# Optimization experiments

Hardware: AMD Instinct MI355X
Metric: run time of the kernel (lower is better)

The kernel has to match this reference:

```python
import jax, jax.numpy as jnp
import numpy as np

N_NODES = 50000
N_EDGES = 500000
N_GRAPH = 128
F_IN = 16
LATENT = 128
STEPS = 3
MLP_LAYERS = 2
OUT_G = 10
LN_EPS = 1e-6


def setup_inputs() -> dict:
    key = jax.random.key(0)
    ks = jax.random.split(key, 8)
    x = jax.random.normal(ks[0], (N_NODES, F_IN), jnp.float32)
    senders = jax.random.randint(ks[1], (N_EDGES,), 0, N_NODES)
    receivers = jax.random.randint(ks[2], (N_EDGES,), 0, N_NODES)
    graph_ids = jnp.sort(jax.random.randint(ks[3], (N_NODES,), 0, N_GRAPH))
    W_embed = jax.random.normal(ks[4], (F_IN, LATENT), jnp.float32) / np.sqrt(F_IN)
    b_embed = jnp.zeros((LATENT,), jnp.float32)
    W_mlp = jax.random.normal(ks[5], (STEPS, MLP_LAYERS, LATENT, LATENT), jnp.float32) / np.sqrt(LATENT)
    b_mlp = jnp.zeros((STEPS, MLP_LAYERS, LATENT), jnp.float32)
    ln_scale = jnp.ones((STEPS, LATENT), jnp.float32)
    ln_bias = jnp.zeros((STEPS, LATENT), jnp.float32)
    W_dec = jax.random.normal(ks[6], (LATENT, OUT_G), jnp.float32) / np.sqrt(LATENT)
    b_dec = jnp.zeros((OUT_G,), jnp.float32)
    return dict(x=x, senders=senders, receivers=receivers, graph_ids=graph_ids,
                W_embed=W_embed, b_embed=b_embed, W_mlp=W_mlp, b_mlp=b_mlp,
                ln_scale=ln_scale, ln_bias=ln_bias, W_dec=W_dec, b_dec=b_dec)


def _layernorm(h, scale, bias):
    mu = jnp.mean(h, axis=-1, keepdims=True)
    var = jnp.mean(jnp.square(h - mu), axis=-1, keepdims=True)
    return (h - mu) * jax.lax.rsqrt(var + LN_EPS) * scale + bias


def reference(x, senders, receivers, graph_ids, W_embed, b_embed,
              W_mlp, b_mlp, ln_scale, ln_bias, W_dec, b_dec):
    N = x.shape[0]
    # node embedder (classical stand-in for quantum node_embedder)
    h = x @ W_embed + b_embed  # [N, latent]

    # add self edges (jraph.GraphConvolution add_self_edges=True)
    self_idx = jnp.arange(N)
    s = jnp.concatenate([senders, self_idx])
    r = jnp.concatenate([receivers, self_idx])
    ones = jnp.ones(s.shape, h.dtype)
    inv_sqrt_deg_s = jax.lax.rsqrt(jnp.maximum(jax.ops.segment_sum(ones, s, N), 1.0))[:, None]
    inv_sqrt_deg_r = jax.lax.rsqrt(jnp.maximum(jax.ops.segment_sum(ones, r, N), 1.0))[:, None]

    for t in range(STEPS):
        # per-node MLP update (Dense + tanh per layer)
        u = h
        for l in range(MLP_LAYERS):
            u = jnp.tanh(u @ W_mlp[t, l] + b_mlp[t, l])
        # symmetric-normalized segment-sum aggregation
        u = u * inv_sqrt_deg_s
        u = jax.ops.segment_sum(u[s], r, N)
        u = u * inv_sqrt_deg_r
        # skip connection + layernorm
        h = u + h
        h = _layernorm(h, ln_scale[t], ln_bias[t])

    # segment-mean pooling over graphs
    counts = jax.ops.segment_sum(jnp.ones((N,), h.dtype), graph_ids, N_GRAPH)
    pooled = jax.ops.segment_sum(h, graph_ids, N_GRAPH) / jnp.maximum(counts, 1.0)[:, None]
    # global decoder
    return pooled @ W_dec + b_dec  # [N_GRAPH, OUT_G]
```

## Files before the change

kernel.cpp:

```cpp
#include <hip/hip_runtime.h>
#include <hip/hip_bf16.h>

#define N_NODES 50000
#define N_EDGES 500000
#define N_GRAPH 128
#define F_IN    16
#define LATENT  128
#define STEPS   3
#define LN_EPS  1e-6f
#define OUT_G   10
#define CAP     48

#define PREP_TOTAL 26428

typedef __attribute__((ext_vector_type(8))) short bf16x8;
typedef __attribute__((ext_vector_type(4))) float f32x4;

__device__ __forceinline__ ushort bf16_rtne(float x) {
    uint u = __float_as_uint(x);
    return (ushort)((u + 0x7FFFu + ((u >> 16) & 1u)) >> 16);
}
__device__ __forceinline__ float bf16_tof(ushort h) {
    return __uint_as_float(((uint)h) << 16);
}
__device__ __forceinline__ float fast_tanh(float x) {
    float t = __expf(x + x);
    return 1.0f - 2.0f * __builtin_amdgcn_rcpf(t + 1.0f);
}

__global__ __launch_bounds__(256) void prep_fused(const int* __restrict__ s,
                                                  const int* __restrict__ r,
                                                  int* __restrict__ cnt_r,
                                                  int* __restrict__ cnt_s,
                                                  ushort* __restrict__ bucket,
                                                  const float* __restrict__ x,
                                                  const float* __restrict__ We,
                                                  const float* __restrict__ be,
                                                  ushort* __restrict__ h_hi,
                                                  ushort* __restrict__ h_lo,
                                                  const float* __restrict__ Wm,
                                                  ushort* __restrict__ w_hi,
                                                  ushort* __restrict__ w_lo,
                                                  const int* __restrict__ gids,
                                                  int* __restrict__ gstart,
                                                  float* __restrict__ pooled) {
    const int bid = blockIdx.x;
    const int tid = threadIdx.x;

    if (bid % 27 == 0) {
        int eidx = bid / 27;
        int e0 = (eidx * 256 + tid) * 2;
        if (e0 < N_EDGES) {
            int2 ss = *reinterpret_cast<const int2*>(&s[e0]);
            int2 rr = *reinterpret_cast<const int2*>(&r[e0]);
            int sl0 = atomicAdd(&cnt_r[rr.x], 1);
            int sl1 = atomicAdd(&cnt_r[rr.y], 1);
            if (sl0 < CAP) bucket[rr.x * CAP + sl0] = (ushort)ss.x;
            if (sl1 < CAP) bucket[rr.y * CAP + sl1] = (ushort)ss.y;
            atomicAdd(&cnt_s[ss.x], 1);
            atomicAdd(&cnt_s[ss.y], 1);
        }
        return;
    }
    int nidx = bid - bid / 27 - 1;

    if (nidx < 25000) {
        int idx = nidx * 256 + tid;
        int n = idx >> 7, j = idx & 127;
        float sacc = be[j];
        #pragma unroll
        for (int k = 0; k < F_IN; ++k) sacc = fmaf(x[n * F_IN + k], We[k * LATENT + j], sacc);
        ushort hi = bf16_rtne(sacc);
        h_hi[idx] = hi;
        h_lo[idx] = bf16_rtne(sacc - bf16_tof(hi));
    } else if (nidx < 25384) {
        int idx = (nidx - 25000) * 256 + tid;
        int tl = idx >> 14, rem = idx & 16383, j = rem >> 7, k = rem & 127;
        float w = Wm[(tl << 14) + k * 128 + j];
        ushort hi = bf16_rtne(w);
        w_hi[idx] = hi;
        w_lo[idx] = bf16_rtne(w - bf16_tof(hi));
    } else if (nidx < 25448) {
        pooled[(nidx - 25384) * 256 + tid] = 0.0f;
    } else {
        if (tid <= N_GRAPH) {
            int lo = 0, hi = N_NODES;
            while (lo < hi) { int m = (lo + hi) >> 1; if (gids[m] < tid) lo = m + 1; else hi = m; }
            gstart[tid] = lo;
        }
    }
}

__global__ __launch_bounds__(256) void deg_fin(const int* __restrict__ cnt_s,
                                               const int* __restrict__ cnt_r,
                                               float* __restrict__ inv_s,
                                               float* __restrict__ inv_r, int N) {
    int i = blockIdx.x * 256 + threadIdx.x;
    if (i < N) {
        inv_s[i] = 1.0f / sqrtf((float)(cnt_s[i] + 1));
        inv_r[i] = 1.0f / sqrtf((float)(cnt_r[i] + 1));
    }
}

__global__ __launch_bounds__(256) void mlp_mfma(const ushort* __restrict__ hsp_hi,
                                                const ushort* __restrict__ hsp_lo,
                                                const ushort* __restrict__ wth,
                                                const ushort* __restrict__ wtl,
                                                const float* __restrict__ b0,
                                                const float* __restrict__ b1,
                                                const float* __restrict__ inv_s,
                                                ushort* __restrict__ v16, int N) {
    __shared__ ushort sh_hi[32][136];
    __shared__ ushort sh_lo[32][136];
    const int tid = threadIdx.x;
    const int base = blockIdx.x * 32;

    #pragma unroll
    for (int it = 0; it < 2; ++it) {
        int chunk = it * 256 + tid;
        int row = chunk >> 4, c8 = (chunk & 15) * 8;
        int node = base + row;
        uint4 dh = make_uint4(0, 0, 0, 0), dl = make_uint4(0, 0, 0, 0);
        if (node < N) {
            dh = *reinterpret_cast<const uint4*>(&hsp_hi[node * 128 + c8]);
            dl = *reinterpret_cast<const uint4*>(&hsp_lo[node * 128 + c8]);
        }
        *reinterpret_cast<uint4*>(&sh_hi[row][c8]) = dh;
        *reinterpret_cast<uint4*>(&sh_lo[row][c8]) = dl;
    }
    __syncthreads();

    const int lane = tid & 63;
    const int wv = tid >> 6;
    const int lrow = lane & 15;
    const int lk = (lane >> 4) * 8;
    const int c0 = wv * 32;
    const int crow0 = (lane >> 4) * 4;

    f32x4 acc[2][2];

    {
        float bb0 = b0[c0 + lrow], bb1 = b0[c0 + 16 + lrow];
        #pragma unroll
        for (int rt = 0; rt < 2; ++rt) {
            acc[rt][0] = (f32x4){bb0, bb0, bb0, bb0};
            acc[rt][1] = (f32x4){bb1, bb1, bb1, bb1};
        }
        #pragma unroll
        for (int kt = 0; kt < 4; ++kt) {
            int kk = kt * 32 + lk;
            bf16x8 bh0 = *reinterpret_cast<const bf16x8*>(&wth[(c0 + lrow) * 128 + kk]);
            bf16x8 bl0 = *reinterpret_cast<const bf16x8*>(&wtl[(c0 + lrow) * 128 + kk]);
            bf16x8 bh1 = *reinterpret_cast<const bf16x8*>(&wth[(c0 + 16 + lrow) * 128 + kk]);
            bf16x8 bl1 = *reinterpret_cast<const bf16x8*>(&wtl[(c0 + 16 + lrow) * 128 + kk]);
            #pragma unroll
            for (int rt = 0; rt < 2; ++rt) {
                bf16x8 ah = *reinterpret_cast<const bf16x8*>(&sh_hi[rt * 16 + lrow][kk]);
                bf16x8 al = *reinterpret_cast<const bf16x8*>(&sh_lo[rt * 16 + lrow][kk]);
                acc[rt][0] = __builtin_amdgcn_mfma_f32_16x16x32_bf16(ah, bh0, acc[rt][0], 0, 0, 0);
                acc[rt][0] = __builtin_amdgcn_mfma_f32_16x16x32_bf16(al, bh0, acc[rt][0], 0, 0, 0);
                acc[rt][0] = __builtin_amdgcn_mfma_f32_16x16x32_bf16(ah, bl0, acc[rt][0], 0, 0, 0);
                acc[rt][1] = __builtin_amdgcn_mfma_f32_16x16x32_bf16(ah, bh1, acc[rt][1], 0, 0, 0);
                acc[rt][1] = __builtin_amdgcn_mfma_f32_16x16x32_bf16(al, bh1, acc[rt][1], 0, 0, 0);
                acc[rt][1] = __builtin_amdgcn_mfma_f32_16x16x32_bf16(ah, bl1, acc[rt][1], 0, 0, 0);
            }
        }
    }
    __syncthreads();

    #pragma unroll
    for (int rt = 0; rt < 2; ++rt) {
        #pragma unroll
        for (int ct = 0; ct < 2; ++ct) {
            int col = c0 + ct * 16 + lrow;
            #pragma unroll
            for (int r = 0; r < 4; ++r) {
                float uval = fast_tanh(acc[rt][ct][r]);
                int row = rt * 16 + crow0 + r;
                ushort uh = bf16_rtne(uval);
                ushort ul = bf16_rtne(uval - bf16_tof(uh));
                sh_hi[row][col] = uh;
                sh_lo[row][col] = ul;
            }
        }
    }
    __syncthreads();

    {
        const ushort* w2h = wth + 128 * 128;
        const ushort* w2l = wtl + 128 * 128;
        float bb0 = b1[c0 + lrow], bb1 = b1[c0 + 16 + lrow];
        #pragma unroll
        for (int rt = 0; rt < 2; ++rt) {
            acc[rt][0] = (f32x4){bb0, bb0, bb0, bb0};
            acc[rt][1] = (f32x4){bb1, bb1, bb1, bb1};
        }
        #pragma unroll
        for (int kt = 0; kt < 4; ++kt) {
            int kk = kt * 32 + lk;
            bf16x8 bh0 = *reinterpret_cast<const bf16x8*>(&w2h[(c0 + lrow) * 128 + kk]);
            bf16x8 bl0 = *reinterpret_cast<const bf16x8*>(&w2l[(c0 + lrow) * 128 + kk]);
            bf16x8 bh1 = *reinterpret_cast<const bf16x8*>(&w2h[(c0 + 16 + lrow) * 128 + kk]);
            bf16x8 bl1 = *reinterpret_cast<const bf16x8*>(&w2l[(c0 + 16 + lrow) * 128 + kk]);
            #pragma unroll
            for (int rt = 0; rt < 2; ++rt) {
                bf16x8 ah = *reinterpret_cast<const bf16x8*>(&sh_hi[rt * 16 + lrow][kk]);
                bf16x8 al = *reinterpret_cast<const bf16x8*>(&sh_lo[rt * 16 + lrow][kk]);
                acc[rt][0] = __builtin_amdgcn_mfma_f32_16x16x32_bf16(ah, bh0, acc[rt][0], 0, 0, 0);
                acc[rt][0] = __builtin_amdgcn_mfma_f32_16x16x32_bf16(al, bh0, acc[rt][0], 0, 0, 0);
                acc[rt][0] = __builtin_amdgcn_mfma_f32_16x16x32_bf16(ah, bl0, acc[rt][0], 0, 0, 0);
                acc[rt][1] = __builtin_amdgcn_mfma_f32_16x16x32_bf16(ah, bh1, acc[rt][1], 0, 0, 0);
                acc[rt][1] = __builtin_amdgcn_mfma_f32_16x16x32_bf16(al, bh1, acc[rt][1], 0, 0, 0);
                acc[rt][1] = __builtin_amdgcn_mfma_f32_16x16x32_bf16(ah, bl1, acc[rt][1], 0, 0, 0);
            }
        }
    }

    #pragma unroll
    for (int rt = 0; rt < 2; ++rt) {
        #pragma unroll
        for (int r = 0; r < 4; ++r) {
            int row = rt * 16 + crow0 + r;
            int node = base + row;
            if (node < N) {
                float is = inv_s[node];
                v16[node * 128 + c0 + lrow]      = bf16_rtne(fast_tanh(acc[rt][0][r]) * is);
                v16[node * 128 + c0 + 16 + lrow] = bf16_rtne(fast_tanh(acc[rt][1][r]) * is);
            }
        }
    }
}

__global__ __launch_bounds__(256) void agg_ln_kernel(const ushort* __restrict__ v16,
                                                     const int* __restrict__ cnt_r,
                                                     const ushort* __restrict__ bucket,
                                                     const float* __restrict__ inv_r,
                                                     const float* __restrict__ ln_scale,
                                                     const float* __restrict__ ln_bias,
                                                     ushort* __restrict__ h_hi,
                                                     ushort* __restrict__ h_lo) {
    int lane = threadIdx.x & 63;
    int wave = threadIdx.x >> 6;
    int n = blockIdx.x * 4 + wave;
    int c0 = lane * 2;

    const uint* vu = reinterpret_cast<const uint*>(v16);

    int deg = cnt_r[n];
    deg = deg < CAP ? deg : CAP;
    const ushort* nbr = bucket + n * CAP;

    float ir = inv_r[n];
    ushort2 hh = *reinterpret_cast<const ushort2*>(&h_hi[n * 128 + c0]);
    ushort2 hl = *reinterpret_cast<const ushort2*>(&h_lo[n * 128 + c0]);
    uint self = vu[n * 64 + lane];
    float2 acc;
    acc.x = bf16_tof((ushort)(self & 0xffffu));
    acc.y = bf16_tof((ushort)(self >> 16));

    {
        int cnt = deg;
        int my = 0;
        if (lane < cnt) my = (int)nbr[lane];
        int k = 0;
        for (; k + 8 <= cnt; k += 8) {
            int s0 = __shfl(my, k + 0), s1 = __shfl(my, k + 1);
            int s2 = __shfl(my, k + 2), s3 = __shfl(my, k + 3);
            int s4 = __shfl(my, k + 4), s5 = __shfl(my, k + 5);
            int s6 = __shfl(my, k + 6), s7 = __shfl(my, k + 7);
            uint t0 = vu[s0 * 64 + lane];
            uint t1 = vu[s1 * 64 + lane];
            uint t2 = vu[s2 * 64 + lane];
            uint t3 = vu[s3 * 64 + lane];
            uint t4 = vu[s4 * 64 + lane];
            uint t5 = vu[s5 * 64 + lane];
            uint t6 = vu[s6 * 64 + lane];
            uint t7 = vu[s7 * 64 + lane];
            acc.x += ((bf16_tof((ushort)(t0 & 0xffffu)) + bf16_tof((ushort)(t1 & 0xffffu)))
                   +  (bf16_tof((ushort)(t2 & 0xffffu)) + bf16_tof((ushort)(t3 & 0xffffu))))
                  + ((bf16_tof((ushort)(t4 & 0xffffu)) + bf16_tof((ushort)(t5 & 0xffffu)))
                   +  (bf16_tof((ushort)(t6 & 0xffffu)) + bf16_tof((ushort)(t7 & 0xffffu))));
            acc.y += ((bf16_tof((ushort)(t0 >> 16)) + bf16_tof((ushort)(t1 >> 16)))
                   +  (bf16_tof((ushort)(t2 >> 16)) + bf16_tof((ushort)(t3 >> 16))))
                  + ((bf16_tof((ushort)(t4 >> 16)) + bf16_tof((ushort)(t5 >> 16)))
                   +  (bf16_tof((ushort)(t6 >> 16)) + bf16_tof((ushort)(t7 >> 16))));
        }
        if (k + 4 <= cnt) {
            int s0 = __shfl(my, k + 0), s1 = __shfl(my, k + 1);
            int s2 = __shfl(my, k + 2), s3 = __shfl(my, k + 3);
            uint t0 = vu[s0 * 64 + lane];
            uint t1 = vu[s1 * 64 + lane];
            uint t2 = vu[s2 * 64 + lane];
            uint t3 = vu[s3 * 64 + lane];
            acc.x += (bf16_tof((ushort)(t0 & 0xffffu)) + bf16_tof((ushort)(t1 & 0xffffu)))
                   + (bf16_tof((ushort)(t2 & 0xffffu)) + bf16_tof((ushort)(t3 & 0xffffu)));
            acc.y += (bf16_tof((ushort)(t0 >> 16)) + bf16_tof((ushort)(t1 >> 16)))
                   + (bf16_tof((ushort)(t2 >> 16)) + bf16_tof((ushort)(t3 >> 16)));
            k += 4;
        }
        for (; k < cnt; ++k) {
            int s = __shfl(my, k);
            uint t = vu[s * 64 + lane];
            acc.x += bf16_tof((ushort)(t & 0xffffu));
            acc.y += bf16_tof((ushort)(t >> 16));
        }
    }

    float hrx = bf16_tof(hh.x) + bf16_tof(hl.x);
    float hry = bf16_tof(hh.y) + bf16_tof(hl.y);
    float vx = fmaf(acc.x, ir, hrx);
    float vy = fmaf(acc.y, ir, hry);

    float sred = vx + vy;
    #pragma unroll
    for (int off = 32; off; off >>= 1) sred += __shfl_xor(sred, off);
    float mu = sred * (1.0f / 128.0f);
    float dx = vx - mu, dy = vy - mu;
    float q = dx * dx + dy * dy;
    #pragma unroll
    for (int off = 32; off; off >>= 1) q += __shfl_xor(q, off);
    float rs = 1.0f / sqrtf(q * (1.0f / 128.0f) + LN_EPS);

    float ox = fmaf(dx * rs, ln_scale[c0],     ln_bias[c0]);
    float oy = fmaf(dy * rs, ln_scale[c0 + 1], ln_bias[c0 + 1]);
    ushort ohx = bf16_rtne(ox), ohy = bf16_rtne(oy);
    ushort olx = bf16_rtne(ox - bf16_tof(ohx)), oly = bf16_rtne(oy - bf16_tof(ohy));
    *reinterpret_cast<ushort2*>(&h_hi[n * 128 + c0]) = make_ushort2(ohx, ohy);
    *reinterpret_cast<ushort2*>(&h_lo[n * 128 + c0]) = make_ushort2(olx, oly);
}

__global__ __launch_bounds__(128) void pool_partial(const ushort* __restrict__ h_hi,
                                                    const ushort* __restrict__ h_lo,
                                                    const int* __restrict__ gstart,
                                                    float* __restrict__ pooled) {
    int g = blockIdx.x >> 3;
    int sidx = blockIdx.x & 7;
    int start = gstart[g], end = gstart[g + 1];
    int len = end - start;
    int c0 = start + (len * sidx) / 8;
    int c1 = start + (len * (sidx + 1)) / 8;
    if (c1 <= c0) return;
    int j = threadIdx.x;
    float sacc = 0.0f;
    for (int n = c0; n < c1; ++n)
        sacc += bf16_tof(h_hi[n * 128 + j]) + bf16_tof(h_lo[n * 128 + j]);
    atomicAdd(&pooled[g * 128 + j], sacc);
}

__global__ __launch_bounds__(128) void decode_kernel(const float* __restrict__ pooled,
                                                     const int* __restrict__ gstart,
                                                     const float* __restrict__ W_dec,
                                                     const float* __restrict__ b_dec,
                                                     float* __restrict__ out) {
    __shared__ float pl[128];
    int g = blockIdx.x;
    int cnt = gstart[g + 1] - gstart[g];
    float inv = 1.0f / (float)max(cnt, 1);
    pl[threadIdx.x] = pooled[g * 128 + threadIdx.x] * inv;
    __syncthreads();
    if (threadIdx.x < OUT_G) {
        int o = threadIdx.x;
        float sacc = b_dec[o];
        for (int jj = 0; jj < 128; ++jj) sacc = fmaf(pl[jj], W_dec[jj * OUT_G + o], sacc);
        out[g * OUT_G + o] = sacc;
    }
}

extern "C" void kernel_launch(void* const* d_in, const int* in_sizes, int n_in,
                              void* d_out, int out_size, void* d_ws, size_t ws_size,
                              hipStream_t stream) {
    const float* x        = (const float*)d_in[0];
    const int*   senders  = (const int*)d_in[1];
    const int*   receivers= (const int*)d_in[2];
    const int*   gids     = (const int*)d_in[3];
    const float* W_embed  = (const float*)d_in[4];
    const float* b_embed  = (const float*)d_in[5];
    const float* W_mlp    = (const float*)d_in[6];
    const float* b_mlp    = (const float*)d_in[7];
    const float* ln_scale = (const float*)d_in[8];
    const float* ln_bias  = (const float*)d_in[9];
    const float* W_dec    = (const float*)d_in[10];
    const float* b_dec    = (const float*)d_in[11];
    float* out = (float*)d_out;

    const int N = N_NODES;
    char* ws = (char*)d_ws;
    size_t off = 0;
    auto alloc = [&](size_t bytes) { size_t o = off; off = (off + bytes + 255) & ~(size_t)255; return o; };
    ushort* h_hi    = (ushort*)(ws + alloc((size_t)N * 128 * 2));
    ushort* h_lo    = (ushort*)(ws + alloc((size_t)N * 128 * 2));
    ushort* v16     = (ushort*)(ws + alloc((size_t)N * 128 * 2));
    int*   cnts     = (int*)  (ws + alloc((size_t)2 * N * 4));
    int*   cnt_r    = cnts;
    int*   cnt_s    = cnts + N;
    float* inv_s    = (float*)(ws + alloc((size_t)N * 4));
    float* inv_r    = (float*)(ws + alloc((size_t)N * 4));
    ushort* bucket  = (ushort*)(ws + alloc((size_t)N * CAP * 2));
    float* pooled   = (float*)(ws + alloc((size_t)N_GRAPH * 128 * 4));
    int*   gstart   = (int*)  (ws + alloc((size_t)(N_GRAPH + 1) * 4));
    ushort* w_hi    = (ushort*)(ws + alloc((size_t)STEPS * 2 * 128 * 128 * 2));
    ushort* w_lo    = (ushort*)(ws + alloc((size_t)STEPS * 2 * 128 * 128 * 2));

    hipMemsetAsync(cnts, 0, (size_t)2 * N * 4, stream);
    prep_fused<<<PREP_TOTAL, 256, 0, stream>>>(senders, receivers, cnt_r, cnt_s, bucket,
                                               x, W_embed, b_embed, h_hi, h_lo,
                                               W_mlp, w_hi, w_lo, gids, gstart, pooled);
    deg_fin<<<(N + 255) / 256, 256, 0, stream>>>(cnt_s, cnt_r, inv_s, inv_r, N);

    for (int t = 0; t < STEPS; ++t) {
        const ushort* wth = w_hi + (size_t)t * 2 * 128 * 128;
        const ushort* wtl = w_lo + (size_t)t * 2 * 128 * 128;
        const float* bb0 = b_mlp + (size_t)(t * 2 + 0) * 128;
        const float* bb1 = b_mlp + (size_t)(t * 2 + 1) * 128;
        mlp_mfma<<<(N + 31) / 32, 256, 0, stream>>>(h_hi, h_lo, wth, wtl, bb0, bb1, inv_s, v16, N);
        agg_ln_kernel<<<N / 4, 256, 0, stream>>>(v16, cnt_r, bucket, inv_r,
                                                 ln_scale + t * 128, ln_bias + t * 128, h_hi, h_lo);
    }

    pool_partial <<<N_GRAPH * 8, 128, 0, stream>>>(h_hi, h_lo, gstart, pooled);
    decode_kernel<<<N_GRAPH, 128, 0, stream>>>(pooled, gstart, W_dec, b_dec, out);
}
```

Measured before the change: 342.6 us.

## Process two nodes per wavefront in aggregation with 8-byte gathers

The aggregation+layernorm kernel now maps two destination nodes to each 64-lane wave, with each half-wave handling one node and each lane covering four channels through 8-byte loads. Neighbor lists are broadcast per half-wave, and a masked tail loop zero-weights gathers from padded slots so both halves can run the same loop despite different degrees. The goal is fewer, wider gather instructions and better memory-level parallelism per wave. In exchange, degree divergence between the paired nodes produces wasted (self-index) gathers, and the reductions now use only 32-lane shuffles.

```diff
diff --git a/kernel.cpp b/kernel.cpp
--- a/kernel.cpp
+++ b/kernel.cpp
@@ -26,6 +26,12 @@
 __device__ __forceinline__ float fast_tanh(float x) {
     float t = __expf(x + x);
     return 1.0f - 2.0f * __builtin_amdgcn_rcpf(t + 1.0f);
+}
+__device__ __forceinline__ void acc4(float4& a, uint2 t, float w) {
+    a.x = fmaf(bf16_tof((ushort)(t.x & 0xffffu)), w, a.x);
+    a.y = fmaf(bf16_tof((ushort)(t.x >> 16)),     w, a.y);
+    a.z = fmaf(bf16_tof((ushort)(t.y & 0xffffu)), w, a.z);
+    a.w = fmaf(bf16_tof((ushort)(t.y >> 16)),     w, a.w);
 }
 
 __global__ __launch_bounds__(256) void prep_fused(const int* __restrict__ s,
@@ -241,92 +247,98 @@
                                                      ushort* __restrict__ h_lo) {
     int lane = threadIdx.x & 63;
     int wave = threadIdx.x >> 6;
-    int n = blockIdx.x * 4 + wave;
-    int c0 = lane * 2;
-
-    const uint* vu = reinterpret_cast<const uint*>(v16);
+    int half = lane >> 5;
+    int l32  = lane & 31;
+    int hb   = lane & 32;
+    int n = blockIdx.x * 8 + wave * 2 + half;
+    int c0 = l32 * 4;
+
+    const uint2* vu2 = reinterpret_cast<const uint2*>(v16);
 
     int deg = cnt_r[n];
     deg = deg < CAP ? deg : CAP;
-    const ushort* nbr = bucket + n * CAP;
+    int degOther = __shfl_xor(deg, 32);
+    int degMin = deg < degOther ? deg : degOther;
+    int degMax = deg > degOther ? deg : degOther;
+
+    int my = (l32 < deg) ? (int)bucket[n * CAP + l32] : n;
 
     float ir = inv_r[n];
-    ushort2 hh = *reinterpret_cast<const ushort2*>(&h_hi[n * 128 + c0]);
-    ushort2 hl = *reinterpret_cast<const ushort2*>(&h_lo[n * 128 + c0]);
-    uint self = vu[n * 64 + lane];
-    float2 acc;
-    acc.x = bf16_tof((ushort)(self & 0xffffu));
-    acc.y = bf16_tof((ushort)(self >> 16));
-
-    {
-        int cnt = deg;
-        int my = 0;
-        if (lane < cnt) my = (int)nbr[lane];
-        int k = 0;
-        for (; k + 8 <= cnt; k += 8) {
-            int s0 = __shfl(my, k + 0), s1 = __shfl(my, k + 1);
-            int s2 = __shfl(my, k + 2), s3 = __shfl(my, k + 3);
-            int s4 = __shfl(my, k + 4), s5 = __shfl(my, k + 5);
-            int s6 = __shfl(my, k + 6), s7 = __shfl(my, k + 7);
-            uint t0 = vu[s0 * 64 + lane];
-            uint t1 = vu[s1 * 64 + lane];
-            uint t2 = vu[s2 * 64 + lane];
-            uint t3 = vu[s3 * 64 + lane];
-            uint t4 = vu[s4 * 64 + lane];
-            uint t5 = vu[s5 * 64 + lane];
-            uint t6 = vu[s6 * 64 + lane];
-            uint t7 = vu[s7 * 64 + lane];
-            acc.x += ((bf16_tof((ushort)(t0 & 0xffffu)) + bf16_tof((ushort)(t1 & 0xffffu)))
-                   +  (bf16_tof((ushort)(t2 & 0xffffu)) + bf16_tof((ushort)(t3 & 0xffffu))))
-                  + ((bf16_tof((ushort)(t4 & 0xffffu)) + bf16_tof((ushort)(t5 & 0xffffu)))
-                   +  (bf16_tof((ushort)(t6 & 0xffffu)) + bf16_tof((ushort)(t7 & 0xffffu))));
-            acc.y += ((bf16_tof((ushort)(t0 >> 16)) + bf16_tof((ushort)(t1 >> 16)))
-                   +  (bf16_tof((ushort)(t2 >> 16)) + bf16_tof((ushort)(t3 >> 16))))
-                  + ((bf16_tof((ushort)(t4 >> 16)) + bf16_tof((ushort)(t5 >> 16)))
-                   +  (bf16_tof((ushort)(t6 >> 16)) + bf16_tof((ushort)(t7 >> 16))));
-        }
-        if (k + 4 <= cnt) {
-            int s0 = __shfl(my, k + 0), s1 = __shfl(my, k + 1);
-            int s2 = __shfl(my, k + 2), s3 = __shfl(my, k + 3);
-            uint t0 = vu[s0 * 64 + lane];
-            uint t1 = vu[s1 * 64 + lane];
-            uint t2 = vu[s2 * 64 + lane];
-            uint t3 = vu[s3 * 64 + lane];
-            acc.x += (bf16_tof((ushort)(t0 & 0xffffu)) + bf16_tof((ushort)(t1 & 0xffffu)))
-                   + (bf16_tof((ushort)(t2 & 0xffffu)) + bf16_tof((ushort)(t3 & 0xffffu)));
-            acc.y += (bf16_tof((ushort)(t0 >> 16)) + bf16_tof((ushort)(t1 >> 16)))
-                   + (bf16_tof((ushort)(t2 >> 16)) + bf16_tof((ushort)(t3 >> 16)));
-            k += 4;
-        }
-        for (; k < cnt; ++k) {
-            int s = __shfl(my, k);
-            uint t = vu[s * 64 + lane];
-            acc.x += bf16_tof((ushort)(t & 0xffffu));
-            acc.y += bf16_tof((ushort)(t >> 16));
-        }
-    }
-
-    float hrx = bf16_tof(hh.x) + bf16_tof(hl.x);
-    float hry = bf16_tof(hh.y) + bf16_tof(hl.y);
-    float vx = fmaf(acc.x, ir, hrx);
-    float vy = fmaf(acc.y, ir, hry);
-
-    float sred = vx + vy;
+    ushort4 hh = *reinterpret_cast<const ushort4*>(&h_hi[n * 128 + c0]);
+    ushort4 hl = *reinterpret_cast<const ushort4*>(&h_lo[n * 128 + c0]);
+    uint2 selfv = vu2[n * 32 + l32];
+    float4 acc = make_float4(0.f, 0.f, 0.f, 0.f);
+    acc4(acc, selfv, 1.0f);
+
+    int dm = degMin < 32 ? degMin : 32;
+    int dx = degMax < 32 ? degMax : 32;
+    int k = 0;
+    for (; k + 8 <= dm; k += 8) {
+        int src[8]; uint2 t[8];
+        #pragma unroll
+        for (int j = 0; j < 8; ++j) src[j] = __shfl(my, hb + k + j);
+        #pragma unroll
+        for (int j = 0; j < 8; ++j) t[j] = vu2[src[j] * 32 + l32];
+        #pragma unroll
+        for (int j = 0; j < 8; ++j) acc4(acc, t[j], 1.0f);
+    }
+    for (; k < dx; k += 8) {
+        int src[8]; uint2 t[8];
+        #pragma unroll
+        for (int j = 0; j < 8; ++j) {
+            int kj = k + j; kj = kj < 31 ? kj : 31;
+            src[j] = __shfl(my, hb + kj);
+        }
+        #pragma unroll
+        for (int j = 0; j < 8; ++j) t[j] = vu2[src[j] * 32 + l32];
+        #pragma unroll
+        for (int j = 0; j < 8; ++j) acc4(acc, t[j], (k + j < deg) ? 1.0f : 0.0f);
+    }
+    if (degMax > 32) {
+        int my2 = (l32 + 32 < deg) ? (int)bucket[n * CAP + 32 + l32] : n;
+        for (int k2 = 32; k2 < degMax; k2 += 8) {
+            int src[8]; uint2 t[8];
+            #pragma unroll
+            for (int j = 0; j < 8; ++j) {
+                int kj = k2 + j - 32; kj = kj < 15 ? kj : 15;
+                src[j] = __shfl(my2, hb + kj);
+            }
+            #pragma unroll
+            for (int j = 0; j < 8; ++j) t[j] = vu2[src[j] * 32 + l32];
+            #pragma unroll
+            for (int j = 0; j < 8; ++j) acc4(acc, t[j], (k2 + j < deg) ? 1.0f : 0.0f);
+        }
+    }
+
+    float4 vv;
+    vv.x = fmaf(acc.x, ir, bf16_tof(hh.x) + bf16_tof(hl.x));
+    vv.y = fmaf(acc.y, ir, bf16_tof(hh.y) + bf16_tof(hl.y));
+    vv.z = fmaf(acc.z, ir, bf16_tof(hh.z) + bf16_tof(hl.z));
+    vv.w = fmaf(acc.w, ir, bf16_tof(hh.w) + bf16_tof(hl.w));
+
+    float sred = (vv.x + vv.y) + (vv.z + vv.w);
     #pragma unroll
-    for (int off = 32; off; off >>= 1) sred += __shfl_xor(sred, off);
+    for (int off = 16; off; off >>= 1) sred += __shfl_xor(sred, off);
     float mu = sred * (1.0f / 128.0f);
-    float dx = vx - mu, dy = vy - mu;
-    float q = dx * dx + dy * dy;
+    float dx0 = vv.x - mu, dy0 = vv.y - mu, dz0 = vv.z - mu, dw0 = vv.w - mu;
+    float q = (dx0 * dx0 + dy0 * dy0) + (dz0 * dz0 + dw0 * dw0);
     #pragma unroll
-    for (int off = 32; off; off >>= 1) q += __shfl_xor(q, off);
+    for (int off = 16; off; off >>= 1) q += __shfl_xor(q, off);
     float rs = 1.0f / sqrtf(q * (1.0f / 128.0f) + LN_EPS);
 
-    float ox = fmaf(dx * rs, ln_scale[c0],     ln_bias[c0]);
-    float oy = fmaf(dy * rs, ln_scale[c0 + 1], ln_bias[c0 + 1]);
-    ushort ohx = bf16_rtne(ox), ohy = bf16_rtne(oy);
-    ushort olx = bf16_rtne(ox - bf16_tof(ohx)), oly = bf16_rtne(oy - bf16_tof(ohy));
-    *reinterpret_cast<ushort2*>(&h_hi[n * 128 + c0]) = make_ushort2(ohx, ohy);
-    *reinterpret_cast<ushort2*>(&h_lo[n * 128 + c0]) = make_ushort2(olx, oly);
+    float4 ls = *reinterpret_cast<const float4*>(&ln_scale[c0]);
+    float4 lb = *reinterpret_cast<const float4*>(&ln_bias[c0]);
+    float o0 = fmaf(dx0 * rs, ls.x, lb.x);
+    float o1 = fmaf(dy0 * rs, ls.y, lb.y);
+    float o2 = fmaf(dz0 * rs, ls.z, lb.z);
+    float o3 = fmaf(dw0 * rs, ls.w, lb.w);
+    ushort h0 = bf16_rtne(o0), h1 = bf16_rtne(o1), h2 = bf16_rtne(o2), h3 = bf16_rtne(o3);
+    ushort l0 = bf16_rtne(o0 - bf16_tof(h0)), l1 = bf16_rtne(o1 - bf16_tof(h1));
+    ushort l2 = bf16_rtne(o2 - bf16_tof(h2)), l3 = bf16_rtne(o3 - bf16_tof(h3));
+    ushort4 oh; oh.x = h0; oh.y = h1; oh.z = h2; oh.w = h3;
+    ushort4 ol; ol.x = l0; ol.y = l1; ol.z = l2; ol.w = l3;
+    *reinterpret_cast<ushort4*>(&h_hi[n * 128 + c0]) = oh;
+    *reinterpret_cast<ushort4*>(&h_lo[n * 128 + c0]) = ol;
 }
 
 __global__ __launch_bounds__(128) void pool_partial(const ushort* __restrict__ h_hi,
@@ -413,7 +425,7 @@
         const float* bb0 = b_mlp + (size_t)(t * 2 + 0) * 128;
         const float* bb1 = b_mlp + (size_t)(t * 2 + 1) * 128;
         mlp_mfma<<<(N + 31) / 32, 256, 0, stream>>>(h_hi, h_lo, wth, wtl, bb0, bb1, inv_s, v16, N);
-        agg_ln_kernel<<<N / 4, 256, 0, stream>>>(v16, cnt_r, bucket, inv_r,
+        agg_ln_kernel<<<N / 8, 256, 0, stream>>>(v16, cnt_r, bucket, inv_r,
                                                  ln_scale + t * 128, ln_bias + t * 128, h_hi, h_lo);
     }
 
```

New measurement: 337.1 us. No clear change (-1.6%).
